# Performance work log

Hardware: AMD Instinct MI355X
Metric: run time of the kernel (lower is better)

The kernel has to match this reference:

```python
import jax, jax.numpy as jnp
import numpy as np

N_NODES = 100000
N_EDGES = 800000
D = 96
BN_EPS = 1e-5
LEAKY_SLOPE = 0.05


def setup_inputs() -> dict:
    key = jax.random.key(0)
    ks = jax.random.split(key, 6)
    node_feat = jax.random.normal(ks[0], (N_NODES, D), dtype=jnp.float32)
    edge_index = jax.random.randint(ks[1], (2, N_EDGES), 0, N_NODES, dtype=jnp.int64)
    W1 = jax.random.normal(ks[2], (D, D), dtype=jnp.float32) / np.sqrt(D)
    b1 = jnp.zeros((D,), dtype=jnp.float32)
    W2 = jax.random.normal(ks[3], (D, D), dtype=jnp.float32) / np.sqrt(D)
    b2 = jnp.zeros((D,), dtype=jnp.float32)
    bn_gamma = jnp.ones((D,), dtype=jnp.float32)
    bn_beta = jnp.zeros((D,), dtype=jnp.float32)
    bn_mean = jnp.zeros((D,), dtype=jnp.float32)
    bn_var = jax.random.uniform(ks[4], (D,), dtype=jnp.float32, minval=0.5, maxval=1.5)
    return {"node_feat": node_feat, "edge_index": edge_index, "W1": W1, "b1": b1,
            "W2": W2, "b2": b2, "bn_gamma": bn_gamma, "bn_beta": bn_beta,
            "bn_mean": bn_mean, "bn_var": bn_var}


def _gcn_norm(edge_index, n_nodes, dtype):
    # add self-loops, symmetric normalization D^{-1/2} (A+I) D^{-1/2}
    loop = jnp.arange(n_nodes, dtype=edge_index.dtype)
    src = jnp.concatenate([edge_index[0], loop])
    dst = jnp.concatenate([edge_index[1], loop])
    deg = jax.ops.segment_sum(jnp.ones(src.shape, dtype=dtype), dst, num_segments=n_nodes)
    dinv = jnp.where(deg > 0, jax.lax.rsqrt(jnp.maximum(deg, 1e-12)), 0.0)
    norm = dinv[src] * dinv[dst]  # [E+N]
    return src, dst, norm


def _gcn_conv(x, W, b, src, dst, norm, n_nodes):
    h = x @ W                              # [N, d_out] dense GEMM
    msg = h[src] * norm[:, None]           # gather + scale, [E+N, d_out]
    agg = jax.ops.segment_sum(msg, dst, num_segments=n_nodes)  # scatter-add
    return agg + b


def reference(node_feat, edge_index, W1, b1, W2, b2, bn_gamma, bn_beta, bn_mean, bn_var):
    n = node_feat.shape[0]
    src, dst, norm = _gcn_norm(edge_index, n, node_feat.dtype)
    # layer 1: GCNConv -> LeakyReLU(0.05) -> BatchNorm1d (eval) -> dropout(eval = identity)
    x = _gcn_conv(node_feat, W1, b1, src, dst, norm, n)
    x = jnp.where(x >= 0, x, LEAKY_SLOPE * x)
    x = (x - bn_mean) * jax.lax.rsqrt(bn_var + BN_EPS) * bn_gamma + bn_beta
    # layer 2 (final): GCNConv only
    x = _gcn_conv(x, W2, b2, src, dst, norm, n)
    return x
```

## Files before the change

kernel.cpp:

```cpp
#include <hip/hip_runtime.h>

#define DF 96
#define BN_EPS 1e-5f
#define SLOPE 0.05f
#define LPN 12
#define GBLK 192
#define NPBG (GBLK / LPN)

typedef __attribute__((ext_vector_type(8))) short bf16x8;
typedef __attribute__((ext_vector_type(4))) float f32x4;
typedef __attribute__((ext_vector_type(8))) unsigned short u16x8;

__device__ __forceinline__ unsigned short f2bf(float f) {
    unsigned u = __builtin_bit_cast(unsigned, f);
    return (unsigned short)((u + 0x7FFFu + ((u >> 16) & 1u)) >> 16);
}
__device__ __forceinline__ float bf2f(unsigned short h) {
    return __builtin_bit_cast(float, (unsigned)h << 16);
}

__global__ __launch_bounds__(256) void k_prep(const float* __restrict__ gamma,
                                              const float* __restrict__ beta,
                                              const float* __restrict__ mean,
                                              const float* __restrict__ var,
                                              float* __restrict__ bnscale,
                                              float* __restrict__ bnbias,
                                              const float* __restrict__ W1,
                                              const float* __restrict__ W2,
                                              unsigned short* __restrict__ Wt1,
                                              unsigned short* __restrict__ Wt2,
                                              int* __restrict__ cnt, int n) {
    int i = blockIdx.x * 256 + threadIdx.x;
    if (i < DF * DF) {
        int nn = i / DF, k = i - nn * DF;
        Wt1[i] = f2bf(W1[k * DF + nn]);
        Wt2[i] = f2bf(W2[k * DF + nn]);
    }
    if (i < DF) {
        float s = gamma[i] * rsqrtf(var[i] + BN_EPS);
        bnscale[i] = s;
        bnbias[i]  = beta[i] - mean[i] * s;
    }
    if (i < n) cnt[i] = 0;
}

__global__ __launch_bounds__(256) void k_countrank(const int* __restrict__ ei,
                                                   int* __restrict__ cnt,
                                                   int* __restrict__ rank, int E) {
    int i = blockIdx.x * 256 + threadIdx.x;
    int e = i * 2;
    if (e + 1 < E) {
        int2 d = *(const int2*)&ei[E + e];
        int r0 = atomicAdd(&cnt[d.x], 1);
        int r1 = atomicAdd(&cnt[d.y], 1);
        *(int2*)&rank[e] = make_int2(r0, r1);
    } else if (e < E) {
        rank[e] = atomicAdd(&cnt[ei[E + e]], 1);
    }
}

__global__ __launch_bounds__(256) void k_scan1(const int* __restrict__ cnt,
                                               int* __restrict__ rowptr,
                                               int* __restrict__ bsum, int n) {
    __shared__ int sh[256];
    int t = threadIdx.x;
    int i = blockIdx.x * 256 + t;
    int x = (i < n) ? cnt[i] : 0;
    sh[t] = x;
    __syncthreads();
#pragma unroll
    for (int off = 1; off < 256; off <<= 1) {
        int v = (t >= off) ? sh[t - off] : 0;
        __syncthreads();
        sh[t] += v;
        __syncthreads();
    }
    if (i < n) rowptr[i] = sh[t] - x;
    if (t == 255) bsum[blockIdx.x] = sh[255];
}

__global__ __launch_bounds__(512) void k_scan23(int* __restrict__ rowptr,
                                                const int* __restrict__ bsum,
                                                const int* __restrict__ cnt,
                                                float* __restrict__ dinv,
                                                int n, int E, int nb) {
    __shared__ int sh[512];
    __shared__ int sbex[512];
    const int t = threadIdx.x;
    int x = (t < nb) ? bsum[t] : 0;
    sh[t] = x;
    __syncthreads();
#pragma unroll
    for (int off = 1; off < 512; off <<= 1) {
        int v = (t >= off) ? sh[t - off] : 0;
        __syncthreads();
        sh[t] += v;
        __syncthreads();
    }
    sbex[t] = sh[t] - x;
    __syncthreads();

    const int i = blockIdx.x * 512 + t;
    if (i < n) {
        rowptr[i] = rowptr[i] + sbex[i >> 8];
        dinv[i]   = rsqrtf((float)cnt[i] + 1.0f);
    }
    if (i == 0) rowptr[n] = E;
}

template <int LAYER>
__device__ __forceinline__ void gemm_body(int bid, int tid, const void* __restrict__ in_,
                                          const unsigned short* __restrict__ Wt,
                                          const float* __restrict__ dinv,
                                          unsigned short* __restrict__ outb, int n) {
    const int wave = tid >> 6;
    const int lane = tid & 63;
    const int l16  = lane & 15;
    const int quad = lane >> 4;
    const int rowbase = bid * 64 + wave * 16;
    const int m = rowbase + l16;
    const bool valid = (m < n);

    bf16x8 bfrag[6][3];
#pragma unroll
    for (int nt = 0; nt < 6; ++nt)
#pragma unroll
        for (int ks = 0; ks < 3; ++ks)
            bfrag[nt][ks] = *(const bf16x8*)&Wt[(nt * 16 + l16) * DF + ks * 32 + quad * 8];

    bf16x8 afrag[3];
    const bf16x8 zf = {};
    if (LAYER == 0) {
        const float* in = (const float*)in_;
        const float* rowp = in + (size_t)m * DF;
        float4 ra[3][2];
#pragma unroll
        for (int ks = 0; ks < 3; ++ks) {
            if (valid) {
                ra[ks][0] = *(const float4*)&rowp[ks * 32 + quad * 8];
                ra[ks][1] = *(const float4*)&rowp[ks * 32 + quad * 8 + 4];
            } else {
                ra[ks][0] = make_float4(0.f, 0.f, 0.f, 0.f);
                ra[ks][1] = make_float4(0.f, 0.f, 0.f, 0.f);
            }
        }
#pragma unroll
        for (int ks = 0; ks < 3; ++ks) {
            const float* a0 = (const float*)&ra[ks][0];
            const float* a1 = (const float*)&ra[ks][1];
            bf16x8 f;
#pragma unroll
            for (int j = 0; j < 4; ++j) {
                f[j]     = (short)f2bf(a0[j]);
                f[j + 4] = (short)f2bf(a1[j]);
            }
            afrag[ks] = f;
        }
    } else {
        const unsigned short* in = (const unsigned short*)in_;
#pragma unroll
        for (int ks = 0; ks < 3; ++ks)
            afrag[ks] = valid ? *(const bf16x8*)&in[(size_t)m * DF + ks * 32 + quad * 8] : zf;
    }

    f32x4 acc[6] = {};
#pragma unroll
    for (int ks = 0; ks < 3; ++ks)
#pragma unroll
        for (int nt = 0; nt < 6; ++nt)
            acc[nt] = __builtin_amdgcn_mfma_f32_16x16x32_bf16(afrag[ks], bfrag[nt][ks],
                                                              acc[nt], 0, 0, 0);

#pragma unroll
    for (int reg = 0; reg < 4; ++reg) {
        const int r = rowbase + quad * 4 + reg;
        if (r < n) {
            const float dv = dinv[r];
#pragma unroll
            for (int nt = 0; nt < 6; ++nt)
                outb[(size_t)r * DF + nt * 16 + l16] = f2bf(acc[nt][reg] * dv);
        }
    }
}

__device__ __forceinline__ void fill_body(int bid, int tid, const int* __restrict__ ei,
                                          const int* __restrict__ rowptr,
                                          const int* __restrict__ rank,
                                          int* __restrict__ csr, int E) {
    int e = bid * 256 + tid;
    if (e < E) {
        int src = ei[e];
        int dst = ei[E + e];
        csr[rowptr[dst] + rank[e]] = src;
    }
}

__global__ __launch_bounds__(256) void k_gemm1_fill(const float* __restrict__ in,
                                                    const unsigned short* __restrict__ Wt1,
                                                    const float* __restrict__ dinv,
                                                    unsigned short* __restrict__ bufA,
                                                    int n, int gb,
                                                    const int* __restrict__ ei,
                                                    const int* __restrict__ rowptr,
                                                    const int* __restrict__ rank,
                                                    int* __restrict__ csr, int E) {
    const int b = blockIdx.x;
    if (b < gb) gemm_body<0>(b, threadIdx.x, in, Wt1, dinv, bufA, n);
    else        fill_body(b - gb, threadIdx.x, ei, rowptr, rank, csr, E);
}

__global__ __launch_bounds__(256) void k_gemm2(const unsigned short* __restrict__ in,
                                               const unsigned short* __restrict__ Wt2,
                                               const float* __restrict__ dinv,
                                               unsigned short* __restrict__ outb, int n) {
    gemm_body<1>(blockIdx.x, threadIdx.x, in, Wt2, dinv, outb, n);
}

template <int LAYER>
__global__ __launch_bounds__(GBLK) void k_gather(const int* __restrict__ rowptr,
                                                 const int* __restrict__ csr,
                                                 const unsigned short* __restrict__ hs,
                                                 const float* __restrict__ dinv,
                                                 const float* __restrict__ b1,
                                                 const float* __restrict__ bnscale,
                                                 const float* __restrict__ bnbias,
                                                 const float* __restrict__ b2,
                                                 void* __restrict__ outp, int n) {
    const int t = threadIdx.x;
    const int v = blockIdx.x * NPBG + t / LPN;
    const int q = t % LPN;
    if (v >= n) return;

    float acc[8];
    {
        const u16x8 h0 = *(const u16x8*)&hs[(size_t)v * DF + q * 8];
#pragma unroll
        for (int i = 0; i < 8; ++i) acc[i] = bf2f(h0[i]);
    }

    const int e0 = rowptr[v];
    const int e1 = rowptr[v + 1];
    int e = e0;
    for (; e + 8 <= e1; e += 8) {
        int s[8];
#pragma unroll
        for (int u = 0; u < 8; ++u) s[u] = csr[e + u];
        u16x8 m[8];
#pragma unroll
        for (int u = 0; u < 8; ++u) m[u] = *(const u16x8*)&hs[(size_t)s[u] * DF + q * 8];
#pragma unroll
        for (int u = 0; u < 8; ++u)
#pragma unroll
            for (int i = 0; i < 8; ++i) acc[i] += bf2f(m[u][i]);
    }
    for (; e + 4 <= e1; e += 4) {
        int s[4];
#pragma unroll
        for (int u = 0; u < 4; ++u) s[u] = csr[e + u];
        u16x8 m[4];
#pragma unroll
        for (int u = 0; u < 4; ++u) m[u] = *(const u16x8*)&hs[(size_t)s[u] * DF + q * 8];
#pragma unroll
        for (int u = 0; u < 4; ++u)
#pragma unroll
            for (int i = 0; i < 8; ++i) acc[i] += bf2f(m[u][i]);
    }
    for (; e < e1; ++e) {
        const int s = csr[e];
        const u16x8 m = *(const u16x8*)&hs[(size_t)s * DF + q * 8];
#pragma unroll
        for (int i = 0; i < 8; ++i) acc[i] += bf2f(m[i]);
    }

    const float dv = dinv[v];
    if (LAYER == 0) {
        u16x8 o;
#pragma unroll
        for (int i = 0; i < 8; ++i) {
            const int c = q * 8 + i;
            float x = __builtin_fmaf(dv, acc[i], b1[c]);
            x = (x >= 0.f) ? x : SLOPE * x;
            o[i] = f2bf(__builtin_fmaf(x, bnscale[c], bnbias[c]));
        }
        *(u16x8*)((unsigned short*)outp + (size_t)v * DF + q * 8) = o;
    } else {
        float* op = (float*)outp + (size_t)v * DF + q * 8;
        float4 o0, o1;
        o0.x = __builtin_fmaf(acc[0], dv, b2[q * 8 + 0]);
        o0.y = __builtin_fmaf(acc[1], dv, b2[q * 8 + 1]);
        o0.z = __builtin_fmaf(acc[2], dv, b2[q * 8 + 2]);
        o0.w = __builtin_fmaf(acc[3], dv, b2[q * 8 + 3]);
        o1.x = __builtin_fmaf(acc[4], dv, b2[q * 8 + 4]);
        o1.y = __builtin_fmaf(acc[5], dv, b2[q * 8 + 5]);
        o1.z = __builtin_fmaf(acc[6], dv, b2[q * 8 + 6]);
        o1.w = __builtin_fmaf(acc[7], dv, b2[q * 8 + 7]);
        *(float4*)op       = o0;
        *(float4*)(op + 4) = o1;
    }
}

extern "C" void kernel_launch(void* const* d_in, const int* in_sizes, int n_in,
                              void* d_out, int out_size, void* d_ws, size_t ws_size,
                              hipStream_t stream) {
    const float* node_feat = (const float*)d_in[0];
    const int*   ei        = (const int*)d_in[1];
    const float* W1        = (const float*)d_in[2];
    const float* b1        = (const float*)d_in[3];
    const float* W2        = (const float*)d_in[4];
    const float* b2        = (const float*)d_in[5];
    const float* gamma     = (const float*)d_in[6];
    const float* beta      = (const float*)d_in[7];
    const float* mean      = (const float*)d_in[8];
    const float* var       = (const float*)d_in[9];

    const int n  = in_sizes[0] / DF;
    const int E  = in_sizes[1] / 2;
    const int nb = (n + 255) / 256;

    char* base = (char*)d_ws;
    size_t off = 0;
    auto alloc = [&](size_t bytes) { void* p = base + off; off = (off + bytes + 15) & ~(size_t)15; return p; };
    int*   cnt     = (int*)alloc(sizeof(int) * n);
    int*   rowptr  = (int*)alloc(sizeof(int) * (n + 1));
    int*   bsum    = (int*)alloc(sizeof(int) * 512);
    float* dinv    = (float*)alloc(sizeof(float) * n);
    float* bnscale = (float*)alloc(sizeof(float) * DF);
    float* bnbias  = (float*)alloc(sizeof(float) * DF);
    unsigned short* Wt1 = (unsigned short*)alloc(sizeof(short) * DF * DF);
    unsigned short* Wt2 = (unsigned short*)alloc(sizeof(short) * DF * DF);
    int*   rank    = (int*)alloc(sizeof(int) * E);
    int*   csr     = (int*)alloc(sizeof(int) * E);
    unsigned short* bufA = (unsigned short*)alloc(sizeof(short) * (size_t)n * DF);
    unsigned short* bufB = (unsigned short*)alloc(sizeof(short) * (size_t)n * DF);
    float* out     = (float*)d_out;

    k_prep<<<nb, 256, 0, stream>>>(gamma, beta, mean, var, bnscale, bnbias,
                                   W1, W2, Wt1, Wt2, cnt, n);
    k_countrank<<<(E / 2 + 255) / 256, 256, 0, stream>>>(ei, cnt, rank, E);
    k_scan1<<<nb, 256, 0, stream>>>(cnt, rowptr, bsum, n);
    k_scan23<<<(n + 511) / 512, 512, 0, stream>>>(rowptr, bsum, cnt, dinv, n, E, nb);

    const int gb = (n + 63) / 64;
    const int fb = (E + 255) / 256;
    const int gagather = (n + NPBG - 1) / NPBG;

    k_gemm1_fill<<<gb + fb, 256, 0, stream>>>(node_feat, Wt1, dinv, bufA, n, gb,
                                              ei, rowptr, rank, csr, E);
    k_gather<0><<<gagather, GBLK, 0, stream>>>(rowptr, csr, bufA, dinv, b1, bnscale,
                                               bnbias, b2, bufB, n);
    k_gemm2<<<gb, 256, 0, stream>>>(bufB, Wt2, dinv, bufA, n);
    k_gather<1><<<gagather, GBLK, 0, stream>>>(rowptr, csr, bufA, dinv, b1, bnscale,
                                               bnbias, b2, out, n);
}
```

Measured before the change: 261.7 us.

## Fuse layer-2 GEMM into layer-1 gather and merge scan kernels

```diff
diff --git a/kernel.cpp b/kernel.cpp
--- a/kernel.cpp
+++ b/kernel.cpp
@@ -6,6 +6,7 @@
 #define LPN 12
 #define GBLK 192
 #define NPBG (GBLK / LPN)
+#define XPAD 104
 
 typedef __attribute__((ext_vector_type(8))) short bf16x8;
 typedef __attribute__((ext_vector_type(4))) float f32x4;
@@ -29,7 +30,8 @@
                                               const float* __restrict__ W2,
                                               unsigned short* __restrict__ Wt1,
                                               unsigned short* __restrict__ Wt2,
-                                              int* __restrict__ cnt, int n) {
+                                              int* __restrict__ cnt,
+                                              int* __restrict__ done, int n) {
     int i = blockIdx.x * 256 + threadIdx.x;
     if (i < DF * DF) {
         int nn = i / DF, k = i - nn * DF;
@@ -41,6 +43,7 @@
         bnscale[i] = s;
         bnbias[i]  = beta[i] - mean[i] * s;
     }
+    if (i == 0) *done = 0;
     if (i < n) cnt[i] = 0;
 }
 
@@ -59,13 +62,17 @@
     }
 }
 
-__global__ __launch_bounds__(256) void k_scan1(const int* __restrict__ cnt,
-                                               int* __restrict__ rowptr,
-                                               int* __restrict__ bsum, int n) {
+__global__ __launch_bounds__(256) void k_scan(const int* __restrict__ cnt,
+                                              int* __restrict__ rowptr,
+                                              int* __restrict__ bsum,
+                                              int* __restrict__ done,
+                                              float* __restrict__ dinv,
+                                              int n, int E, int nb) {
     __shared__ int sh[256];
-    int t = threadIdx.x;
-    int i = blockIdx.x * 256 + t;
-    int x = (i < n) ? cnt[i] : 0;
+    const int t = threadIdx.x;
+    const int b = blockIdx.x;
+    const int i = b * 256 + t;
+    const int x = (i < n) ? cnt[i] : 0;
     sh[t] = x;
     __syncthreads();
 #pragma unroll
@@ -75,44 +82,41 @@
         sh[t] += v;
         __syncthreads();
     }
-    if (i < n) rowptr[i] = sh[t] - x;
-    if (t == 255) bsum[blockIdx.x] = sh[255];
-}
-
-__global__ __launch_bounds__(512) void k_scan23(int* __restrict__ rowptr,
-                                                const int* __restrict__ bsum,
-                                                const int* __restrict__ cnt,
-                                                float* __restrict__ dinv,
-                                                int n, int E, int nb) {
-    __shared__ int sh[512];
-    __shared__ int sbex[512];
-    const int t = threadIdx.x;
-    int x = (t < nb) ? bsum[t] : 0;
-    sh[t] = x;
+    const int incl = sh[t];
+    if (t == 255) {
+        bsum[b] = incl;
+        __threadfence();
+        atomicAdd(done, 1);
+    }
+    if (t == 0) {
+        while (__hip_atomic_load(done, __ATOMIC_ACQUIRE, __HIP_MEMORY_SCOPE_AGENT) < nb) {}
+    }
     __syncthreads();
-#pragma unroll
-    for (int off = 1; off < 512; off <<= 1) {
-        int v = (t >= off) ? sh[t - off] : 0;
+    __threadfence();
+
+    int part = 0;
+    for (int j = t; j < b; j += 256) part += bsum[j];
+    __syncthreads();
+    sh[t] = part;
+    __syncthreads();
+#pragma unroll
+    for (int s = 128; s > 0; s >>= 1) {
+        if (t < s) sh[t] += sh[t + s];
         __syncthreads();
-        sh[t] += v;
-        __syncthreads();
-    }
-    sbex[t] = sh[t] - x;
-    __syncthreads();
-
-    const int i = blockIdx.x * 512 + t;
+    }
+    const int offset = sh[0];
+
     if (i < n) {
-        rowptr[i] = rowptr[i] + sbex[i >> 8];
-        dinv[i]   = rsqrtf((float)cnt[i] + 1.0f);
+        rowptr[i] = offset + incl - x;
+        dinv[i]   = rsqrtf((float)x + 1.0f);
     }
     if (i == 0) rowptr[n] = E;
 }
 
-template <int LAYER>
-__device__ __forceinline__ void gemm_body(int bid, int tid, const void* __restrict__ in_,
-                                          const unsigned short* __restrict__ Wt,
-                                          const float* __restrict__ dinv,
-                                          unsigned short* __restrict__ outb, int n) {
+__device__ __forceinline__ void gemm1_body(int bid, int tid, const float* __restrict__ in,
+                                           const unsigned short* __restrict__ Wt,
+                                           const float* __restrict__ dinv,
+                                           unsigned short* __restrict__ outb, int n) {
     const int wave = tid >> 6;
     const int lane = tid & 63;
     const int l16  = lane & 15;
@@ -128,39 +132,30 @@
         for (int ks = 0; ks < 3; ++ks)
             bfrag[nt][ks] = *(const bf16x8*)&Wt[(nt * 16 + l16) * DF + ks * 32 + quad * 8];
 
+    const float* rowp = in + (size_t)m * DF;
+    float4 ra[3][2];
+#pragma unroll
+    for (int ks = 0; ks < 3; ++ks) {
+        if (valid) {
+            ra[ks][0] = *(const float4*)&rowp[ks * 32 + quad * 8];
+            ra[ks][1] = *(const float4*)&rowp[ks * 32 + quad * 8 + 4];
+        } else {
+            ra[ks][0] = make_float4(0.f, 0.f, 0.f, 0.f);
+            ra[ks][1] = make_float4(0.f, 0.f, 0.f, 0.f);
+        }
+    }
     bf16x8 afrag[3];
-    const bf16x8 zf = {};
-    if (LAYER == 0) {
-        const float* in = (const float*)in_;
-        const float* rowp = in + (size_t)m * DF;
-        float4 ra[3][2];
-#pragma unroll
-        for (int ks = 0; ks < 3; ++ks) {
-            if (valid) {
-                ra[ks][0] = *(const float4*)&rowp[ks * 32 + quad * 8];
-                ra[ks][1] = *(const float4*)&rowp[ks * 32 + quad * 8 + 4];
-            } else {
-                ra[ks][0] = make_float4(0.f, 0.f, 0.f, 0.f);
-                ra[ks][1] = make_float4(0.f, 0.f, 0.f, 0.f);
-            }
-        }
-#pragma unroll
-        for (int ks = 0; ks < 3; ++ks) {
-            const float* a0 = (const float*)&ra[ks][0];
-            const float* a1 = (const float*)&ra[ks][1];
-            bf16x8 f;
-#pragma unroll
-            for (int j = 0; j < 4; ++j) {
-                f[j]     = (short)f2bf(a0[j]);
-                f[j + 4] = (short)f2bf(a1[j]);
-            }
-            afrag[ks] = f;
-        }
-    } else {
-        const unsigned short* in = (const unsigned short*)in_;
-#pragma unroll
-        for (int ks = 0; ks < 3; ++ks)
-            afrag[ks] = valid ? *(const bf16x8*)&in[(size_t)m * DF + ks * 32 + quad * 8] : zf;
+#pragma unroll
+    for (int ks = 0; ks < 3; ++ks) {
+        const float* a0 = (const float*)&ra[ks][0];
+        const float* a1 = (const float*)&ra[ks][1];
+        bf16x8 f;
+#pragma unroll
+        for (int j = 0; j < 4; ++j) {
+            f[j]     = (short)f2bf(a0[j]);
+            f[j + 4] = (short)f2bf(a1[j]);
+        }
+        afrag[ks] = f;
     }
 
     f32x4 acc[6] = {};
@@ -205,75 +200,67 @@
                                                     const int* __restrict__ rank,
                                                     int* __restrict__ csr, int E) {
     const int b = blockIdx.x;
-    if (b < gb) gemm_body<0>(b, threadIdx.x, in, Wt1, dinv, bufA, n);
+    if (b < gb) gemm1_body(b, threadIdx.x, in, Wt1, dinv, bufA, n);
     else        fill_body(b - gb, threadIdx.x, ei, rowptr, rank, csr, E);
 }
 
-__global__ __launch_bounds__(256) void k_gemm2(const unsigned short* __restrict__ in,
-                                               const unsigned short* __restrict__ Wt2,
-                                               const float* __restrict__ dinv,
-                                               unsigned short* __restrict__ outb, int n) {
-    gemm_body<1>(blockIdx.x, threadIdx.x, in, Wt2, dinv, outb, n);
-}
-
-template <int LAYER>
-__global__ __launch_bounds__(GBLK) void k_gather(const int* __restrict__ rowptr,
-                                                 const int* __restrict__ csr,
-                                                 const unsigned short* __restrict__ hs,
-                                                 const float* __restrict__ dinv,
-                                                 const float* __restrict__ b1,
-                                                 const float* __restrict__ bnscale,
-                                                 const float* __restrict__ bnbias,
-                                                 const float* __restrict__ b2,
-                                                 void* __restrict__ outp, int n) {
-    const int t = threadIdx.x;
-    const int v = blockIdx.x * NPBG + t / LPN;
-    const int q = t % LPN;
-    if (v >= n) return;
-
-    float acc[8];
-    {
-        const u16x8 h0 = *(const u16x8*)&hs[(size_t)v * DF + q * 8];
-#pragma unroll
-        for (int i = 0; i < 8; ++i) acc[i] = bf2f(h0[i]);
-    }
-
-    const int e0 = rowptr[v];
-    const int e1 = rowptr[v + 1];
-    int e = e0;
-    for (; e + 8 <= e1; e += 8) {
-        int s[8];
-#pragma unroll
-        for (int u = 0; u < 8; ++u) s[u] = csr[e + u];
-        u16x8 m[8];
-#pragma unroll
-        for (int u = 0; u < 8; ++u) m[u] = *(const u16x8*)&hs[(size_t)s[u] * DF + q * 8];
-#pragma unroll
-        for (int u = 0; u < 8; ++u)
-#pragma unroll
-            for (int i = 0; i < 8; ++i) acc[i] += bf2f(m[u][i]);
-    }
-    for (; e + 4 <= e1; e += 4) {
-        int s[4];
-#pragma unroll
-        for (int u = 0; u < 4; ++u) s[u] = csr[e + u];
-        u16x8 m[4];
-#pragma unroll
-        for (int u = 0; u < 4; ++u) m[u] = *(const u16x8*)&hs[(size_t)s[u] * DF + q * 8];
-#pragma unroll
-        for (int u = 0; u < 4; ++u)
-#pragma unroll
-            for (int i = 0; i < 8; ++i) acc[i] += bf2f(m[u][i]);
-    }
-    for (; e < e1; ++e) {
-        const int s = csr[e];
-        const u16x8 m = *(const u16x8*)&hs[(size_t)s * DF + q * 8];
-#pragma unroll
-        for (int i = 0; i < 8; ++i) acc[i] += bf2f(m[i]);
-    }
-
-    const float dv = dinv[v];
-    if (LAYER == 0) {
+__global__ __launch_bounds__(GBLK) void k_gather0_gemm2(const int* __restrict__ rowptr,
+                                                        const int* __restrict__ csr,
+                                                        const unsigned short* __restrict__ hs,
+                                                        const float* __restrict__ dinv,
+                                                        const float* __restrict__ b1,
+                                                        const float* __restrict__ bnscale,
+                                                        const float* __restrict__ bnbias,
+                                                        const unsigned short* __restrict__ Wt2,
+                                                        unsigned short* __restrict__ outb,
+                                                        int n) {
+    __shared__ unsigned short sx[NPBG * XPAD];
+    const int t  = threadIdx.x;
+    const int vl = t / LPN;
+    const int q  = t % LPN;
+    const int v  = blockIdx.x * NPBG + vl;
+
+    if (v < n) {
+        float acc[8];
+        {
+            const u16x8 h0 = *(const u16x8*)&hs[(size_t)v * DF + q * 8];
+#pragma unroll
+            for (int i = 0; i < 8; ++i) acc[i] = bf2f(h0[i]);
+        }
+        const int e1 = rowptr[v + 1];
+        int e = rowptr[v];
+        for (; e + 8 <= e1; e += 8) {
+            int s[8];
+#pragma unroll
+            for (int u = 0; u < 8; ++u) s[u] = csr[e + u];
+            u16x8 m[8];
+#pragma unroll
+            for (int u = 0; u < 8; ++u) m[u] = *(const u16x8*)&hs[(size_t)s[u] * DF + q * 8];
+#pragma unroll
+            for (int u = 0; u < 8; ++u)
+#pragma unroll
+                for (int i = 0; i < 8; ++i) acc[i] += bf2f(m[u][i]);
+        }
+        for (; e + 4 <= e1; e += 4) {
+            int s[4];
+#pragma unroll
+            for (int u = 0; u < 4; ++u) s[u] = csr[e + u];
+            u16x8 m[4];
+#pragma unroll
+            for (int u = 0; u < 4; ++u) m[u] = *(const u16x8*)&hs[(size_t)s[u] * DF + q * 8];
+#pragma unroll
+            for (int u = 0; u < 4; ++u)
+#pragma unroll
+                for (int i = 0; i < 8; ++i) acc[i] += bf2f(m[u][i]);
+        }
+        for (; e < e1; ++e) {
+            const int s = csr[e];
+            const u16x8 m = *(const u16x8*)&hs[(size_t)s * DF + q * 8];
+#pragma unroll
+            for (int i = 0; i < 8; ++i) acc[i] += bf2f(m[i]);
+        }
+
+        const float dv = dinv[v];
         u16x8 o;
 #pragma unroll
         for (int i = 0; i < 8; ++i) {
@@ -282,21 +269,110 @@
             x = (x >= 0.f) ? x : SLOPE * x;
             o[i] = f2bf(__builtin_fmaf(x, bnscale[c], bnbias[c]));
         }
-        *(u16x8*)((unsigned short*)outp + (size_t)v * DF + q * 8) = o;
-    } else {
-        float* op = (float*)outp + (size_t)v * DF + q * 8;
-        float4 o0, o1;
-        o0.x = __builtin_fmaf(acc[0], dv, b2[q * 8 + 0]);
-        o0.y = __builtin_fmaf(acc[1], dv, b2[q * 8 + 1]);
-        o0.z = __builtin_fmaf(acc[2], dv, b2[q * 8 + 2]);
-        o0.w = __builtin_fmaf(acc[3], dv, b2[q * 8 + 3]);
-        o1.x = __builtin_fmaf(acc[4], dv, b2[q * 8 + 4]);
-        o1.y = __builtin_fmaf(acc[5], dv, b2[q * 8 + 5]);
-        o1.z = __builtin_fmaf(acc[6], dv, b2[q * 8 + 6]);
-        o1.w = __builtin_fmaf(acc[7], dv, b2[q * 8 + 7]);
-        *(float4*)op       = o0;
-        *(float4*)(op + 4) = o1;
-    }
+        *(u16x8*)&sx[vl * XPAD + q * 8] = o;
+    }
+    __syncthreads();
+
+    if (t < 64) {
+        const int l16  = t & 15;
+        const int quad = t >> 4;
+        bf16x8 afrag[3];
+#pragma unroll
+        for (int ks = 0; ks < 3; ++ks)
+            afrag[ks] = *(const bf16x8*)&sx[l16 * XPAD + ks * 32 + quad * 8];
+
+        bf16x8 bfrag[6][3];
+#pragma unroll
+        for (int nt = 0; nt < 6; ++nt)
+#pragma unroll
+            for (int ks = 0; ks < 3; ++ks)
+                bfrag[nt][ks] = *(const bf16x8*)&Wt2[(nt * 16 + l16) * DF + ks * 32 + quad * 8];
+
+        f32x4 acc2[6] = {};
+#pragma unroll
+        for (int ks = 0; ks < 3; ++ks)
+#pragma unroll
+            for (int nt = 0; nt < 6; ++nt)
+                acc2[nt] = __builtin_amdgcn_mfma_f32_16x16x32_bf16(afrag[ks], bfrag[nt][ks],
+                                                                   acc2[nt], 0, 0, 0);
+
+        const int rowbase = blockIdx.x * NPBG;
+#pragma unroll
+        for (int reg = 0; reg < 4; ++reg) {
+            const int r = rowbase + quad * 4 + reg;
+            if (r < n) {
+                const float dv = dinv[r];
+#pragma unroll
+                for (int nt = 0; nt < 6; ++nt)
+                    outb[(size_t)r * DF + nt * 16 + l16] = f2bf(acc2[nt][reg] * dv);
+            }
+        }
+    }
+}
+
+__global__ __launch_bounds__(GBLK) void k_gather_final(const int* __restrict__ rowptr,
+                                                       const int* __restrict__ csr,
+                                                       const unsigned short* __restrict__ hs,
+                                                       const float* __restrict__ dinv,
+                                                       const float* __restrict__ b2,
+                                                       float* __restrict__ outp, int n) {
+    const int t = threadIdx.x;
+    const int v = blockIdx.x * NPBG + t / LPN;
+    const int q = t % LPN;
+    if (v >= n) return;
+
+    float acc[8];
+    {
+        const u16x8 h0 = *(const u16x8*)&hs[(size_t)v * DF + q * 8];
+#pragma unroll
+        for (int i = 0; i < 8; ++i) acc[i] = bf2f(h0[i]);
+    }
+    const int e1 = rowptr[v + 1];
+    int e = rowptr[v];
+    for (; e + 8 <= e1; e += 8) {
+        int s[8];
+#pragma unroll
+        for (int u = 0; u < 8; ++u) s[u] = csr[e + u];
+        u16x8 m[8];
+#pragma unroll
+        for (int u = 0; u < 8; ++u) m[u] = *(const u16x8*)&hs[(size_t)s[u] * DF + q * 8];
+#pragma unroll
+        for (int u = 0; u < 8; ++u)
+#pragma unroll
+            for (int i = 0; i < 8; ++i) acc[i] += bf2f(m[u][i]);
+    }
+    for (; e + 4 <= e1; e += 4) {
+        int s[4];
+#pragma unroll
+        for (int u = 0; u < 4; ++u) s[u] = csr[e + u];
+        u16x8 m[4];
+#pragma unroll
+        for (int u = 0; u < 4; ++u) m[u] = *(const u16x8*)&hs[(size_t)s[u] * DF + q * 8];
+#pragma unroll
+        for (int u = 0; u < 4; ++u)
+#pragma unroll
+            for (int i = 0; i < 8; ++i) acc[i] += bf2f(m[u][i]);
+    }
+    for (; e < e1; ++e) {
+        const int s = csr[e];
+        const u16x8 m = *(const u16x8*)&hs[(size_t)s * DF + q * 8];
+#pragma unroll
+        for (int i = 0; i < 8; ++i) acc[i] += bf2f(m[i]);
+    }
+
+    const float dv = dinv[v];
+    float* op = (float*)outp + (size_t)v * DF + q * 8;
+    float4 o0, o1;
+    o0.x = __builtin_fmaf(acc[0], dv, b2[q * 8 + 0]);
+    o0.y = __builtin_fmaf(acc[1], dv, b2[q * 8 + 1]);
+    o0.z = __builtin_fmaf(acc[2], dv, b2[q * 8 + 2]);
+    o0.w = __builtin_fmaf(acc[3], dv, b2[q * 8 + 3]);
+    o1.x = __builtin_fmaf(acc[4], dv, b2[q * 8 + 4]);
+    o1.y = __builtin_fmaf(acc[5], dv, b2[q * 8 + 5]);
+    o1.z = __builtin_fmaf(acc[6], dv, b2[q * 8 + 6]);
+    o1.w = __builtin_fmaf(acc[7], dv, b2[q * 8 + 7]);
+    *(float4*)op       = o0;
+    *(float4*)(op + 4) = o1;
 }
 
 extern "C" void kernel_launch(void* const* d_in, const int* in_sizes, int n_in,
@@ -323,6 +399,7 @@
     int*   cnt     = (int*)alloc(sizeof(int) * n);
     int*   rowptr  = (int*)alloc(sizeof(int) * (n + 1));
     int*   bsum    = (int*)alloc(sizeof(int) * 512);
+    int*   done    = (int*)alloc(sizeof(int) * 16);
     float* dinv    = (float*)alloc(sizeof(float) * n);
     float* bnscale = (float*)alloc(sizeof(float) * DF);
     float* bnbias  = (float*)alloc(sizeof(float) * DF);
@@ -335,20 +412,17 @@
     float* out     = (float*)d_out;
 
     k_prep<<<nb, 256, 0, stream>>>(gamma, beta, mean, var, bnscale, bnbias,
-                                   W1, W2, Wt1, Wt2, cnt, n);
+                                   W1, W2, Wt1, Wt2, cnt, done, n);
     k_countrank<<<(E / 2 + 255) / 256, 256, 0, stream>>>(ei, cnt, rank, E);
-    k_scan1<<<nb, 256, 0, stream>>>(cnt, rowptr, bsum, n);
-    k_scan23<<<(n + 511) / 512, 512, 0, stream>>>(rowptr, bsum, cnt, dinv, n, E, nb);
+    k_scan<<<nb, 256, 0, stream>>>(cnt, rowptr, bsum, done, dinv, n, E, nb);
 
     const int gb = (n + 63) / 64;
     const int fb = (E + 255) / 256;
-    const int gagather = (n + NPBG - 1) / NPBG;
+    const int gg = (n + NPBG - 1) / NPBG;
 
     k_gemm1_fill<<<gb + fb, 256, 0, stream>>>(node_feat, Wt1, dinv, bufA, n, gb,
                                               ei, rowptr, rank, csr, E);
-    k_gather<0><<<gagather, GBLK, 0, stream>>>(rowptr, csr, bufA, dinv, b1, bnscale,
-                                               bnbias, b2, bufB, n);
-    k_gemm2<<<gb, 256, 0, stream>>>(bufB, Wt2, dinv, bufA, n);
-    k_gather<1><<<gagather, GBLK, 0, stream>>>(rowptr, csr, bufA, dinv, b1, bnscale,
-                                               bnbias, b2, out, n);
-}
+    k_gather0_gemm2<<<gg, GBLK, 0, stream>>>(rowptr, csr, bufA, dinv, b1, bnscale,
+                                             bnbias, Wt2, bufB, n);
+    k_gather_final<<<gg, GBLK, 0, stream>>>(rowptr, csr, bufB, dinv, b2, out, n);
+}
```

After: 307.2 us. 17.4% more time.
